# Kernel tuning notes

Hardware: AMD Instinct MI355X
Metric: run time of the kernel (lower is better)

## Reference

```python
import jax, jax.numpy as jnp
import numpy as np

N_NODES = 100000
N_EDGES = 1600000
D_FEAT = 128
NUM_UNITS = 128


def setup_inputs() -> dict:
    key = jax.random.key(0)
    k1, k2, k3, k4, k5 = jax.random.split(key, 5)
    H = jax.random.normal(k1, (N_NODES, D_FEAT), dtype=jnp.float32)
    edge_vals = jax.random.uniform(k2, (N_EDGES,), dtype=jnp.float32)
    W = jax.random.normal(k3, (D_FEAT, NUM_UNITS), dtype=jnp.float32) / np.sqrt(D_FEAT)
    b = jnp.zeros((NUM_UNITS,), dtype=jnp.float32)
    edge_src = jax.random.randint(k4, (N_EDGES,), 0, N_NODES, dtype=jnp.int32)
    edge_dst = jax.random.randint(k5, (N_EDGES,), 0, N_NODES, dtype=jnp.int32)
    return {"H": H, "edge_vals": edge_vals, "W": W, "b": b,
            "edge_src": edge_src, "edge_dst": edge_dst}


def reference(H, edge_vals, W, b, edge_src, edge_dst):
    # SpMM: AH[i] = sum_{e: src[e]==i} val[e] * H[dst[e]]
    gathered = edge_vals[:, None] * H[edge_dst]            # [E, F]
    AH = jax.ops.segment_sum(gathered, edge_src, num_segments=N_NODES)  # [N, F]
    # Dense projection + bias + relu (tf.layers.Dense with tf.nn.relu)
    return jax.nn.relu(AH @ W + b)
```

## Files before the change

kernel.cpp:

```cpp
#include <hip/hip_runtime.h>

#define N_NODES  100000
#define N_EDGES  1600000
#define D        128
#define NFB      3125
#define SUBCAP   768
#define OCAP     8192
#define FCHUNK   8192
#define FILL_BLOCKS ((N_EDGES + FCHUNK - 1) / FCHUNK)
#define NPACK    ((NFB + 1) / 2)
#define NCUR     (NFB + 3)

typedef __attribute__((ext_vector_type(8))) short bf16x8;
typedef __attribute__((ext_vector_type(4))) float f32x4;

__device__ __forceinline__ unsigned short f2bf(float x) {
    unsigned u = __float_as_uint(x);
    u += 0x7fffu + ((u >> 16) & 1u);
    return (unsigned short)(u >> 16);
}

__global__ __launch_bounds__(256) void init_kernel(
    const float* __restrict__ W, unsigned short* __restrict__ Wfrag,
    int* __restrict__ ccursor)
{
    int t = blockIdx.x * 256 + threadIdx.x;
    if (t <= NCUR) ccursor[t] = 0;
    int k = t >> 7, n = t & 127;
    int c = n >> 4, cc = n & 15, ks = k >> 5, g = (k >> 3) & 3, j = k & 7;
    int lane = g * 16 + cc;
    Wfrag[(size_t)(((c * 4 + ks) * 64) + lane) * 8 + j] = f2bf(W[t]);
}

__global__ __launch_bounds__(1024) void fill_fine(
    const int* __restrict__ src, const int* __restrict__ dst,
    const float* __restrict__ vals, int* __restrict__ ccursor,
    int2* __restrict__ sedge, int4* __restrict__ oflow,
    int* __restrict__ oflow_cnt)
{
    __shared__ unsigned lhistP[NPACK];
    __shared__ unsigned lbaseP[NPACK];
    const int t = threadIdx.x;

    for (int i = t; i < NPACK; i += 1024) lhistP[i] = 0;
    __syncthreads();
    const int e0 = blockIdx.x * FCHUNK;
    const int e1 = min(e0 + FCHUNK, N_EDGES);

    int myS[8]; int myD[8]; float myV[8];
#pragma unroll
    for (int q = 0; q < 8; ++q) {
        int e = e0 + t + q * 1024;
        myS[q] = -1;
        if (e < e1) {
            int s = src[e];
            myS[q] = s;
            myD[q] = dst[e];
            myV[q] = vals[e];
            int b = s >> 5;
            atomicAdd(&lhistP[b >> 1], 1u << ((b & 1) << 4));
        }
    }
    __syncthreads();
    for (int i = t; i < NPACK; i += 1024) {
        unsigned p = lhistP[i];
        unsigned c0 = p & 0xffffu, c1 = p >> 16;
        unsigned b0 = c0 ? (unsigned)atomicAdd(&ccursor[2 * i], (int)c0) : 0u;
        unsigned b1 = c1 ? (unsigned)atomicAdd(&ccursor[2 * i + 1], (int)c1) : 0u;
        lbaseP[i] = (b0 & 0xffffu) | (b1 << 16);
        lhistP[i] = 0;
    }
    __syncthreads();
#pragma unroll
    for (int q = 0; q < 8; ++q) {
        if (myS[q] >= 0) {
            int s = myS[q];
            int b = s >> 5;
            unsigned sh = (unsigned)(b & 1) << 4;
            unsigned old = atomicAdd(&lhistP[b >> 1], 1u << sh);
            int pos = (int)((lbaseP[b >> 1] >> sh) & 0xffffu) +
                      (int)((old >> sh) & 0xffffu);
            if (pos < SUBCAP) {
                int2 p;
                p.x = myD[q] | ((s & 31) << 17);
                p.y = __float_as_int(myV[q]);
                sedge[(size_t)b * SUBCAP + pos] = p;
            } else {
                int oc = atomicAdd(oflow_cnt, 1);
                if (oc < OCAP) oflow[oc] = make_int4(s, myD[q], __float_as_int(myV[q]), 0);
            }
        }
    }
}

__global__ __launch_bounds__(256) void gemm_mfma(
    const float* __restrict__ H, const unsigned short* __restrict__ Wfrag,
    unsigned short* __restrict__ HWb)
{
    const int wid  = threadIdx.x >> 6;
    const int lane = threadIdx.x & 63;
    const int row16 = blockIdx.x * 64 + wid * 16;
    const int g = lane >> 4;

    int arow = row16 + (lane & 15);
    if (arow >= N_NODES) arow = N_NODES - 1;

    f32x4 acc[8];
#pragma unroll
    for (int c = 0; c < 8; ++c) acc[c] = (f32x4){0.f, 0.f, 0.f, 0.f};

#pragma unroll
    for (int ks = 0; ks < 4; ++ks) {
        const float* ap = H + (size_t)arow * D + ks * 32 + g * 8;
        float4 a0 = *reinterpret_cast<const float4*>(ap);
        float4 a1 = *reinterpret_cast<const float4*>(ap + 4);
        bf16x8 af;
        af[0] = (short)f2bf(a0.x); af[1] = (short)f2bf(a0.y);
        af[2] = (short)f2bf(a0.z); af[3] = (short)f2bf(a0.w);
        af[4] = (short)f2bf(a1.x); af[5] = (short)f2bf(a1.y);
        af[6] = (short)f2bf(a1.z); af[7] = (short)f2bf(a1.w);
#pragma unroll
        for (int c = 0; c < 8; ++c) {
            bf16x8 bf = *reinterpret_cast<const bf16x8*>(
                Wfrag + (size_t)((c * 4 + ks) * 64 + lane) * 8);
            acc[c] = __builtin_amdgcn_mfma_f32_16x16x32_bf16(af, bf, acc[c], 0, 0, 0);
        }
    }

#pragma unroll
    for (int c = 0; c < 8; ++c) {
#pragma unroll
        for (int r = 0; r < 4; ++r) {
            int orow = row16 + g * 4 + r;
            if (orow < N_NODES)
                HWb[(size_t)orow * D + c * 16 + (lane & 15)] = f2bf(acc[c][r]);
        }
    }
}

__global__ __launch_bounds__(256) void sort_gather(
    const unsigned short* __restrict__ HWb, const int2* __restrict__ sedge,
    const int* __restrict__ ccursor, const int4* __restrict__ oflow,
    const int* __restrict__ oflow_cnt, const float* __restrict__ bias,
    float* __restrict__ out)
{
    __shared__ int2 eLds[SUBCAP];
    __shared__ int h[32];
    __shared__ int ex[32];
    __shared__ int cur[32];
    const int bkt = blockIdx.x;
    const int t = threadIdx.x;
    const size_t base = (size_t)bkt * SUBCAP;
    const int cnt = min(ccursor[bkt], SUBCAP);

    if (t < 32) h[t] = 0;
    __syncthreads();

    int2 myE[3]; int myR[3];
#pragma unroll
    for (int q = 0; q < 3; ++q) {
        int j = t + q * 256;
        myR[q] = -1;
        if (j < cnt) {
            myE[q] = sedge[base + j];
            myR[q] = (myE[q].x >> 17) & 31;
            atomicAdd(&h[myR[q]], 1);
        }
    }
    __syncthreads();
    if (t < 32) {
        int v = h[t];
        int x = v;
        for (int off = 1; off < 32; off <<= 1) {
            int y = __shfl_up(x, off);
            if (t >= off) x += y;
        }
        ex[t] = x - v;
        cur[t] = 0;
    }
    __syncthreads();
#pragma unroll
    for (int q = 0; q < 3; ++q) {
        if (myR[q] >= 0) {
            int pos = ex[myR[q]] + atomicAdd(&cur[myR[q]], 1);
            int2 e;
            e.x = myE[q].x & 0x1FFFF;
            e.y = myE[q].y;
            eLds[pos] = e;
        }
    }
    __syncthreads();

    const int wid = t >> 6, lane = t & 63;
    const int ovc = *oflow_cnt;
    const float2 bv = *reinterpret_cast<const float2*>(bias + lane * 2);
    for (int ln = wid; ln < 32; ln += 4) {
        int node = bkt * 32 + ln;
        const int j0 = ex[ln], j1 = ex[ln] + h[ln];
        float ax = 0.f, ay = 0.f, bx = 0.f, by = 0.f;
        float cx = 0.f, cy = 0.f, dx = 0.f, dy = 0.f;
        int j = j0;
        for (; j + 4 <= j1; j += 4) {
            int2 e0 = eLds[j],     e1 = eLds[j + 1];
            int2 e2 = eLds[j + 2], e3 = eLds[j + 3];
            unsigned u0 = *reinterpret_cast<const unsigned*>(HWb + (size_t)e0.x * D + lane * 2);
            unsigned u1 = *reinterpret_cast<const unsigned*>(HWb + (size_t)e1.x * D + lane * 2);
            unsigned u2 = *reinterpret_cast<const unsigned*>(HWb + (size_t)e2.x * D + lane * 2);
            unsigned u3 = *reinterpret_cast<const unsigned*>(HWb + (size_t)e3.x * D + lane * 2);
            float v0 = __int_as_float(e0.y), v1 = __int_as_float(e1.y);
            float v2 = __int_as_float(e2.y), v3 = __int_as_float(e3.y);
            ax += v0 * __uint_as_float(u0 << 16);
            ay += v0 * __uint_as_float(u0 & 0xffff0000u);
            bx += v1 * __uint_as_float(u1 << 16);
            by += v1 * __uint_as_float(u1 & 0xffff0000u);
            cx += v2 * __uint_as_float(u2 << 16);
            cy += v2 * __uint_as_float(u2 & 0xffff0000u);
            dx += v3 * __uint_as_float(u3 << 16);
            dy += v3 * __uint_as_float(u3 & 0xffff0000u);
        }
        for (; j < j1; ++j) {
            int2 e = eLds[j];
            unsigned u = *reinterpret_cast<const unsigned*>(HWb + (size_t)e.x * D + lane * 2);
            float v = __int_as_float(e.y);
            ax += v * __uint_as_float(u << 16);
            ay += v * __uint_as_float(u & 0xffff0000u);
        }
        for (int q = 0; q < ovc; ++q) {
            int4 e = oflow[q];
            if (e.x == node) {
                unsigned u = *reinterpret_cast<const unsigned*>(HWb + (size_t)e.y * D + lane * 2);
                float v = __int_as_float(e.z);
                ax += v * __uint_as_float(u << 16);
                ay += v * __uint_as_float(u & 0xffff0000u);
            }
        }
        float2 o;
        o.x = fmaxf((ax + bx) + (cx + dx) + bv.x, 0.f);
        o.y = fmaxf((ay + by) + (cy + dy) + bv.y, 0.f);
        *reinterpret_cast<float2*>(out + (size_t)node * D + lane * 2) = o;
    }
}

extern "C" void kernel_launch(void* const* d_in, const int* in_sizes, int n_in,
                              void* d_out, int out_size, void* d_ws, size_t ws_size,
                              hipStream_t stream) {
    const float* H    = (const float*)d_in[0];
    const float* vals = (const float*)d_in[1];
    const float* W    = (const float*)d_in[2];
    const float* b    = (const float*)d_in[3];
    const int*   src  = (const int*)d_in[4];
    const int*   dst  = (const int*)d_in[5];
    float* out = (float*)d_out;

    unsigned short* HWb   = (unsigned short*)d_ws;
    unsigned short* Wfrag = HWb + (size_t)N_NODES * D;
    int2* sedge     = (int2*)(Wfrag + 128 * 128);
    int*  ccursor   = (int*)(sedge + (size_t)NFB * SUBCAP);
    int*  oflow_cnt = ccursor + NCUR;
    int4* oflow     = (int4*)(((uintptr_t)(oflow_cnt + 1) + 15) & ~(uintptr_t)15);

    init_kernel<<<64, 256, 0, stream>>>(W, Wfrag, ccursor);
    fill_fine<<<FILL_BLOCKS, 1024, 0, stream>>>(src, dst, vals, ccursor,
                                                sedge, oflow, oflow_cnt);
    gemm_mfma<<<(N_NODES + 63) / 64, 256, 0, stream>>>(H, Wfrag, HWb);
    sort_gather<<<NFB, 256, 0, stream>>>(HWb, sedge, ccursor, oflow,
                                         oflow_cnt, b, out);
}
```

Before: 122.0 us.

## Retune block sizes, double rows per GEMM wave, use packed bf16 convert

fill_fine now uses 4096-edge chunks with 512 threads, and sort_gather uses 128 threads, with each wave handling more nodes and more edges per thread. The GEMM gives each wave 32 rows through two accumulator sets, so each W fragment load is reused twice, and it converts H to bf16 with the v_cvt_pk_bf16_f32 instruction. The goal is less per-block overhead, better W reuse, and fewer conversion instructions. The costs are higher register pressure in the GEMM, fewer waves per block for latency hiding in the gather, and more global cursor atomics because the fill uses twice as many blocks.

```diff
diff --git a/kernel.cpp b/kernel.cpp
--- a/kernel.cpp
+++ b/kernel.cpp
@@ -6,18 +6,25 @@
 #define NFB      3125
 #define SUBCAP   768
 #define OCAP     8192
-#define FCHUNK   8192
+#define FCHUNK   4096
 #define FILL_BLOCKS ((N_EDGES + FCHUNK - 1) / FCHUNK)
 #define NPACK    ((NFB + 1) / 2)
 #define NCUR     (NFB + 3)
 
 typedef __attribute__((ext_vector_type(8))) short bf16x8;
 typedef __attribute__((ext_vector_type(4))) float f32x4;
+typedef __attribute__((ext_vector_type(4))) unsigned u32x4;
 
 __device__ __forceinline__ unsigned short f2bf(float x) {
     unsigned u = __float_as_uint(x);
     u += 0x7fffu + ((u >> 16) & 1u);
     return (unsigned short)(u >> 16);
+}
+
+__device__ __forceinline__ unsigned cvt_pk_bf16(float lo, float hi) {
+    unsigned r;
+    asm("v_cvt_pk_bf16_f32 %0, %1, %2" : "=v"(r) : "v"(lo), "v"(hi));
+    return r;
 }
 
 __global__ __launch_bounds__(256) void init_kernel(
@@ -32,7 +39,7 @@
     Wfrag[(size_t)(((c * 4 + ks) * 64) + lane) * 8 + j] = f2bf(W[t]);
 }
 
-__global__ __launch_bounds__(1024) void fill_fine(
+__global__ __launch_bounds__(512) void fill_fine(
     const int* __restrict__ src, const int* __restrict__ dst,
     const float* __restrict__ vals, int* __restrict__ ccursor,
     int2* __restrict__ sedge, int4* __restrict__ oflow,
@@ -42,7 +49,7 @@
     __shared__ unsigned lbaseP[NPACK];
     const int t = threadIdx.x;
 
-    for (int i = t; i < NPACK; i += 1024) lhistP[i] = 0;
+    for (int i = t; i < NPACK; i += 512) lhistP[i] = 0;
     __syncthreads();
     const int e0 = blockIdx.x * FCHUNK;
     const int e1 = min(e0 + FCHUNK, N_EDGES);
@@ -50,7 +57,7 @@
     int myS[8]; int myD[8]; float myV[8];
 #pragma unroll
     for (int q = 0; q < 8; ++q) {
-        int e = e0 + t + q * 1024;
+        int e = e0 + t + q * 512;
         myS[q] = -1;
         if (e < e1) {
             int s = src[e];
@@ -62,7 +69,7 @@
         }
     }
     __syncthreads();
-    for (int i = t; i < NPACK; i += 1024) {
+    for (int i = t; i < NPACK; i += 512) {
         unsigned p = lhistP[i];
         unsigned c0 = p & 0xffffu, c1 = p >> 16;
         unsigned b0 = c0 ? (unsigned)atomicAdd(&ccursor[2 * i], (int)c0) : 0u;
@@ -99,31 +106,40 @@
 {
     const int wid  = threadIdx.x >> 6;
     const int lane = threadIdx.x & 63;
-    const int row16 = blockIdx.x * 64 + wid * 16;
+    const int rowbase = blockIdx.x * 128 + wid * 32;
     const int g = lane >> 4;
 
-    int arow = row16 + (lane & 15);
-    if (arow >= N_NODES) arow = N_NODES - 1;
-
-    f32x4 acc[8];
-#pragma unroll
-    for (int c = 0; c < 8; ++c) acc[c] = (f32x4){0.f, 0.f, 0.f, 0.f};
+    int arow0 = rowbase + (lane & 15);
+    int arow1 = rowbase + 16 + (lane & 15);
+    if (arow0 >= N_NODES) arow0 = N_NODES - 1;
+    if (arow1 >= N_NODES) arow1 = N_NODES - 1;
+
+    f32x4 acc0[8], acc1[8];
+#pragma unroll
+    for (int c = 0; c < 8; ++c) {
+        acc0[c] = (f32x4){0.f, 0.f, 0.f, 0.f};
+        acc1[c] = (f32x4){0.f, 0.f, 0.f, 0.f};
+    }
 
 #pragma unroll
     for (int ks = 0; ks < 4; ++ks) {
-        const float* ap = H + (size_t)arow * D + ks * 32 + g * 8;
-        float4 a0 = *reinterpret_cast<const float4*>(ap);
-        float4 a1 = *reinterpret_cast<const float4*>(ap + 4);
-        bf16x8 af;
-        af[0] = (short)f2bf(a0.x); af[1] = (short)f2bf(a0.y);
-        af[2] = (short)f2bf(a0.z); af[3] = (short)f2bf(a0.w);
-        af[4] = (short)f2bf(a1.x); af[5] = (short)f2bf(a1.y);
-        af[6] = (short)f2bf(a1.z); af[7] = (short)f2bf(a1.w);
+        const float* ap0 = H + (size_t)arow0 * D + ks * 32 + g * 8;
+        const float* ap1 = H + (size_t)arow1 * D + ks * 32 + g * 8;
+        float4 a00 = *reinterpret_cast<const float4*>(ap0);
+        float4 a01 = *reinterpret_cast<const float4*>(ap0 + 4);
+        float4 a10 = *reinterpret_cast<const float4*>(ap1);
+        float4 a11 = *reinterpret_cast<const float4*>(ap1 + 4);
+        union { bf16x8 v; u32x4 u; } af0, af1;
+        af0.u = (u32x4){cvt_pk_bf16(a00.x, a00.y), cvt_pk_bf16(a00.z, a00.w),
+                        cvt_pk_bf16(a01.x, a01.y), cvt_pk_bf16(a01.z, a01.w)};
+        af1.u = (u32x4){cvt_pk_bf16(a10.x, a10.y), cvt_pk_bf16(a10.z, a10.w),
+                        cvt_pk_bf16(a11.x, a11.y), cvt_pk_bf16(a11.z, a11.w)};
 #pragma unroll
         for (int c = 0; c < 8; ++c) {
             bf16x8 bf = *reinterpret_cast<const bf16x8*>(
                 Wfrag + (size_t)((c * 4 + ks) * 64 + lane) * 8);
-            acc[c] = __builtin_amdgcn_mfma_f32_16x16x32_bf16(af, bf, acc[c], 0, 0, 0);
+            acc0[c] = __builtin_amdgcn_mfma_f32_16x16x32_bf16(af0.v, bf, acc0[c], 0, 0, 0);
+            acc1[c] = __builtin_amdgcn_mfma_f32_16x16x32_bf16(af1.v, bf, acc1[c], 0, 0, 0);
         }
     }
 
@@ -131,14 +147,17 @@
     for (int c = 0; c < 8; ++c) {
 #pragma unroll
         for (int r = 0; r < 4; ++r) {
-            int orow = row16 + g * 4 + r;
-            if (orow < N_NODES)
-                HWb[(size_t)orow * D + c * 16 + (lane & 15)] = f2bf(acc[c][r]);
-        }
-    }
-}
-
-__global__ __launch_bounds__(256) void sort_gather(
+            int orow0 = rowbase + g * 4 + r;
+            int orow1 = rowbase + 16 + g * 4 + r;
+            if (orow0 < N_NODES)
+                HWb[(size_t)orow0 * D + c * 16 + (lane & 15)] = f2bf(acc0[c][r]);
+            if (orow1 < N_NODES)
+                HWb[(size_t)orow1 * D + c * 16 + (lane & 15)] = f2bf(acc1[c][r]);
+        }
+    }
+}
+
+__global__ __launch_bounds__(128) void sort_gather(
     const unsigned short* __restrict__ HWb, const int2* __restrict__ sedge,
     const int* __restrict__ ccursor, const int4* __restrict__ oflow,
     const int* __restrict__ oflow_cnt, const float* __restrict__ bias,
@@ -156,10 +175,10 @@
     if (t < 32) h[t] = 0;
     __syncthreads();
 
-    int2 myE[3]; int myR[3];
-#pragma unroll
-    for (int q = 0; q < 3; ++q) {
-        int j = t + q * 256;
+    int2 myE[6]; int myR[6];
+#pragma unroll
+    for (int q = 0; q < 6; ++q) {
+        int j = t + q * 128;
         myR[q] = -1;
         if (j < cnt) {
             myE[q] = sedge[base + j];
@@ -180,7 +199,7 @@
     }
     __syncthreads();
 #pragma unroll
-    for (int q = 0; q < 3; ++q) {
+    for (int q = 0; q < 6; ++q) {
         if (myR[q] >= 0) {
             int pos = ex[myR[q]] + atomicAdd(&cur[myR[q]], 1);
             int2 e;
@@ -194,7 +213,7 @@
     const int wid = t >> 6, lane = t & 63;
     const int ovc = *oflow_cnt;
     const float2 bv = *reinterpret_cast<const float2*>(bias + lane * 2);
-    for (int ln = wid; ln < 32; ln += 4) {
+    for (int ln = wid; ln < 32; ln += 2) {
         int node = bkt * 32 + ln;
         const int j0 = ex[ln], j1 = ex[ln] + h[ln];
         float ax = 0.f, ay = 0.f, bx = 0.f, by = 0.f;
@@ -260,9 +279,9 @@
     int4* oflow     = (int4*)(((uintptr_t)(oflow_cnt + 1) + 15) & ~(uintptr_t)15);
 
     init_kernel<<<64, 256, 0, stream>>>(W, Wfrag, ccursor);
-    fill_fine<<<FILL_BLOCKS, 1024, 0, stream>>>(src, dst, vals, ccursor,
-                                                sedge, oflow, oflow_cnt);
-    gemm_mfma<<<(N_NODES + 63) / 64, 256, 0, stream>>>(H, Wfrag, HWb);
-    sort_gather<<<NFB, 256, 0, stream>>>(HWb, sedge, ccursor, oflow,
+    fill_fine<<<FILL_BLOCKS, 512, 0, stream>>>(src, dst, vals, ccursor,
+                                               sedge, oflow, oflow_cnt);
+    gemm_mfma<<<(N_NODES + 127) / 128, 256, 0, stream>>>(H, Wfrag, HWb);
+    sort_gather<<<NFB, 128, 0, stream>>>(HWb, sedge, ccursor, oflow,
                                          oflow_cnt, b, out);
 }
```

New measurement: 155.6 us. +27.5%, slower.
